# Optimization experiments

Hardware: AMD Instinct MI355X
Metric: run time of the kernel (lower is better)

## Reference

```python
import jax, jax.numpy as jnp
import numpy as np

B = 16384
OUT = 128          # output_size (per conditioning frame)
NCOND = 3
HID = 32           # MLP3 hidden
LSTM_H = 64        # lstm_output_size (input == hidden)
NPRED = 25
EPS = 1e-5


def setup_inputs() -> dict:
    key = jax.random.key(0)
    ks = jax.random.split(key, 20)
    d = {
        "x0": jax.random.normal(ks[0], (B, OUT), jnp.float32),
        "x1": jax.random.normal(ks[1], (B, OUT), jnp.float32),
        "x2": jax.random.normal(ks[2], (B, OUT), jnp.float32),
        # MLP3: Linear(384->32), BN, ReLU, Linear(32->32), BN, ReLU, Linear(32->64)
        "W1": jax.random.normal(ks[3], (HID, OUT * NCOND), jnp.float32) * 0.05,
        "b1": jnp.full((HID,), 0.03, jnp.float32),
        "g1": jnp.ones((HID,), jnp.float32),
        "beta1": jnp.zeros((HID,), jnp.float32),
        "W2": jax.random.normal(ks[4], (HID, HID), jnp.float32) * 0.1,
        "b2": jnp.full((HID,), 0.03, jnp.float32),
        "g2": jnp.ones((HID,), jnp.float32),
        "beta2": jnp.zeros((HID,), jnp.float32),
        "W3": jax.random.normal(ks[5], (LSTM_H, HID), jnp.float32) * 0.1,
        "b3": jnp.full((LSTM_H,), 0.03, jnp.float32),
        # LSTM (torch gate order i,f,g,o): weight_ih (4H,H), weight_hh (4H,H)
        "Wih": jax.random.normal(ks[6], (4 * LSTM_H, LSTM_H), jnp.float32) * 0.08,
        "Whh": jax.random.normal(ks[7], (4 * LSTM_H, LSTM_H), jnp.float32) * 0.08,
        "bih": jnp.zeros((4 * LSTM_H,), jnp.float32),
        "bhh": jnp.zeros((4 * LSTM_H,), jnp.float32),
    }
    return d


def _bn_train(h, g, b):
    # BatchNorm1d in training mode: biased batch statistics
    m = jnp.mean(h, axis=0)
    v = jnp.var(h, axis=0)
    return g * (h - m) * jax.lax.rsqrt(v + EPS) + b


def _lstm_step(inp, h, c, Wih, Whh, bih, bhh):
    gates = inp @ Wih.T + bih + h @ Whh.T + bhh  # (B, 4H)
    i, f, g, o = jnp.split(gates, 4, axis=1)
    c_new = jax.nn.sigmoid(f) * c + jax.nn.sigmoid(i) * jnp.tanh(g)
    h_new = jax.nn.sigmoid(o) * jnp.tanh(c_new)
    return h_new, c_new


def reference(x0, x1, x2, W1, b1, g1, beta1, W2, b2, g2, beta2, W3, b3,
              Wih, Whh, bih, bhh):
    x = jnp.concatenate([x0, x1, x2], axis=1)          # (B, 384)
    h = jax.nn.relu(_bn_train(x @ W1.T + b1, g1, beta1))
    h = jax.nn.relu(_bn_train(h @ W2.T + b2, g2, beta2))
    m = h @ W3.T + b3                                   # (B, 64)

    h0 = jnp.zeros((m.shape[0], LSTM_H), m.dtype)
    c0 = jnp.zeros_like(h0)
    # initial conditioning step (output discarded except as state/next input)
    h1, c1 = _lstm_step(m, h0, c0, Wih, Whh, bih, bhh)

    def step(carry, _):
        hh, cc = carry
        # loop feeds previous output back as input; output == h for 1-layer LSTM
        hn, cn = _lstm_step(hh, hh, cc, Wih, Whh, bih, bhh)
        return (hn, cn), hn

    _, outs = jax.lax.scan(step, (h1, c1), None, length=NPRED)  # (25, B, 64)
    return jnp.transpose(outs, (1, 0, 2))                        # (B, 25, 64)
```

## Files before the change

kernel.cpp:

```cpp
#include <hip/hip_runtime.h>


#define EPSV 1e-5f
#define LOG2E 1.4426950408889634f
#define K2    2.8853900817779268f

typedef __attribute__((ext_vector_type(8))) short bf16x8;
typedef __attribute__((ext_vector_type(4))) float f32x4;

__device__ __forceinline__ float rcp_f(float x) { return __builtin_amdgcn_rcpf(x); }
__device__ __forceinline__ void split_bf16(float x, ushort& hi, ushort& lo) {
    unsigned xb = __builtin_bit_cast(unsigned, x);
    hi = (ushort)(xb >> 16);
    float hif = __builtin_bit_cast(float, xb & 0xffff0000u);
    unsigned lb = __builtin_bit_cast(unsigned, x - hif);
    lo = (ushort)(lb >> 16);
}

__global__ __launch_bounds__(256) void k_prep(
    const float* __restrict__ Wih, const float* __restrict__ Whh,
    const float* __restrict__ bih, const float* __restrict__ bhh,
    const float* __restrict__ W1, const float* __restrict__ W2,
    ushort* __restrict__ Wih_hi, ushort* __restrict__ Wih_lo,
    ushort* __restrict__ Wsum_hi, ushort* __restrict__ Wsum_lo,
    ushort* __restrict__ W1hi, ushort* __restrict__ W1lo,
    ushort* __restrict__ W2hi, ushort* __restrict__ W2lo,
    float* __restrict__ bsum)
{
    int i = blockIdx.x * 256 + threadIdx.x;
    ushort h, l;
    if (i < 16384) {
        int j = i >> 6;
        float sc = (j >= 128 && j < 192) ? K2 : LOG2E;
        float wi  = Wih[i] * sc;
        float wsv = (Wih[i] + Whh[i]) * sc;
        split_bf16(wi, h, l);  Wih_hi[i] = h;  Wih_lo[i] = l;
        split_bf16(wsv, h, l); Wsum_hi[i] = h; Wsum_lo[i] = l;
    }
    if (i < 12288) { split_bf16(W1[i], h, l); W1hi[i] = h; W1lo[i] = l; }
    if (i < 1024)  { split_bf16(W2[i], h, l); W2hi[i] = h; W2lo[i] = l; }
    if (i < 256) {
        float sc = (i >= 128 && i < 192) ? K2 : LOG2E;
        bsum[i] = (bih[i] + bhh[i]) * sc;
    }
}

__global__ __launch_bounds__(256) void k_red(const float* __restrict__ part,
                                             const float* __restrict__ g,
                                             const float* __restrict__ be,
                                             float* __restrict__ scsh) {
    __shared__ float rs[256], rq[256];
    const int ch = blockIdx.x, t = threadIdx.x;
    float s = (part[t * 32 + ch] + part[(t + 256) * 32 + ch]) +
              (part[(t + 512) * 32 + ch] + part[(t + 768) * 32 + ch]);
    float q = (part[32768 + t * 32 + ch] + part[32768 + (t + 256) * 32 + ch]) +
              (part[32768 + (t + 512) * 32 + ch] + part[32768 + (t + 768) * 32 + ch]);
    rs[t] = s; rq[t] = q;
    __syncthreads();
    #pragma unroll
    for (int off = 128; off > 0; off >>= 1) {
        if (t < off) { rs[t] += rs[t + off]; rq[t] += rq[t + off]; }
        __syncthreads();
    }
    if (t == 0) {
        float mu = rs[0] * (1.f / 16384.f);
        float va = rq[0] * (1.f / 16384.f) - mu * mu;
        float sc = g[ch] * rsqrtf(va + EPSV);
        scsh[ch] = sc; scsh[32 + ch] = be[ch] - mu * sc;
    }
}

__global__ __launch_bounds__(256) void k_mlp1(
    const float* __restrict__ x0, const float* __restrict__ x1, const float* __restrict__ x2,
    const ushort* __restrict__ W1hi, const ushort* __restrict__ W1lo,
    const float* __restrict__ b1,
    float* __restrict__ pre, float* __restrict__ st1p)
{
    __shared__ __align__(16) ushort xhi[32 * 392];
    __shared__ __align__(16) ushort xlo[32 * 392];
    const int tid = threadIdx.x;
    const int r0  = blockIdx.x * 32;

    for (int a = 0; a < 3; ++a) {
        const float* xp = (a == 0) ? x0 : (a == 1) ? x1 : x2;
        const float4* src = (const float4*)(xp + (size_t)r0 * 128);
        #pragma unroll
        for (int it = 0; it < 4; ++it) {
            int i = it * 256 + tid;
            int row = i >> 5, c4 = i & 31;
            float4 v = src[i];
            ushort h0, l0, h1, l1, h2, l2, h3, l3;
            split_bf16(v.x, h0, l0); split_bf16(v.y, h1, l1);
            split_bf16(v.z, h2, l2); split_bf16(v.w, h3, l3);
            int ofs = row * 392 + a * 128 + c4 * 4;
            *(ushort4*)&xhi[ofs] = make_ushort4(h0, h1, h2, h3);
            *(ushort4*)&xlo[ofs] = make_ushort4(l0, l1, l2, l3);
        }
    }
    __syncthreads();

    const int lane = tid & 63, l15 = lane & 15, lg = lane >> 4, q = tid >> 6;
    const int m0 = (q & 1) * 16, n0 = (q >> 1) * 16;
    const float bias = b1[n0 + l15];
    f32x4 acc = {bias, bias, bias, bias};
    #pragma unroll
    for (int kt = 0; kt < 12; ++kt) {
        bf16x8 ahi = *(const bf16x8*)&xhi[(m0 + l15) * 392 + kt * 32 + lg * 8];
        bf16x8 alo = *(const bf16x8*)&xlo[(m0 + l15) * 392 + kt * 32 + lg * 8];
        bf16x8 bhi = *(const bf16x8*)(W1hi + (size_t)(n0 + l15) * 384 + kt * 32 + lg * 8);
        bf16x8 blo = *(const bf16x8*)(W1lo + (size_t)(n0 + l15) * 384 + kt * 32 + lg * 8);
        acc = __builtin_amdgcn_mfma_f32_16x16x32_bf16(ahi, bhi, acc, 0, 0, 0);
        acc = __builtin_amdgcn_mfma_f32_16x16x32_bf16(ahi, blo, acc, 0, 0, 0);
        acc = __builtin_amdgcn_mfma_f32_16x16x32_bf16(alo, bhi, acc, 0, 0, 0);
    }
    #pragma unroll
    for (int rg = 0; rg < 4; ++rg)
        pre[(size_t)(r0 + m0 + lg * 4 + rg) * 32 + n0 + l15] = acc[rg];
    float s  = (acc[0] + acc[1]) + (acc[2] + acc[3]);
    float sq = (acc[0] * acc[0] + acc[1] * acc[1]) + (acc[2] * acc[2] + acc[3] * acc[3]);
    s  += __shfl_xor(s, 16);  s  += __shfl_xor(s, 32);
    sq += __shfl_xor(sq, 16); sq += __shfl_xor(sq, 32);
    if (lg == 0) {
        int slot = (blockIdx.x * 2 + (q & 1)) * 32 + n0 + l15;
        st1p[slot] = s;
        st1p[32768 + slot] = sq;
    }
}

__global__ __launch_bounds__(256) void k_mlp2(
    float* __restrict__ pre, const float* __restrict__ scsh1,
    const ushort* __restrict__ W2hi, const ushort* __restrict__ W2lo,
    const float* __restrict__ b2, float* __restrict__ st2p)
{
    __shared__ __align__(16) ushort hhi[32 * 40];
    __shared__ __align__(16) ushort hlo[32 * 40];
    __shared__ float bnsc[32], bnsh[32];
    const int tid = threadIdx.x;
    const int r0  = blockIdx.x * 32;

    if (tid < 32) { bnsc[tid] = scsh1[tid]; bnsh[tid] = scsh1[32 + tid]; }
    __syncthreads();
    {
        int row = tid >> 3, c4 = tid & 7;
        float4 v = ((const float4*)(pre + (size_t)r0 * 32))[tid];
        float e0 = fmaxf(fmaf(v.x, bnsc[c4 * 4 + 0], bnsh[c4 * 4 + 0]), 0.f);
        float e1 = fmaxf(fmaf(v.y, bnsc[c4 * 4 + 1], bnsh[c4 * 4 + 1]), 0.f);
        float e2 = fmaxf(fmaf(v.z, bnsc[c4 * 4 + 2], bnsh[c4 * 4 + 2]), 0.f);
        float e3 = fmaxf(fmaf(v.w, bnsc[c4 * 4 + 3], bnsh[c4 * 4 + 3]), 0.f);
        ushort h0, l0, h1, l1, h2, l2, h3, l3;
        split_bf16(e0, h0, l0); split_bf16(e1, h1, l1);
        split_bf16(e2, h2, l2); split_bf16(e3, h3, l3);
        int ofs = row * 40 + c4 * 4;
        *(ushort4*)&hhi[ofs] = make_ushort4(h0, h1, h2, h3);
        *(ushort4*)&hlo[ofs] = make_ushort4(l0, l1, l2, l3);
    }
    __syncthreads();

    const int lane = tid & 63, l15 = lane & 15, lg = lane >> 4, q = tid >> 6;
    const int m0 = (q & 1) * 16, n0 = (q >> 1) * 16;
    const float bias = b2[n0 + l15];
    f32x4 acc = {bias, bias, bias, bias};
    bf16x8 ahi = *(const bf16x8*)&hhi[(m0 + l15) * 40 + lg * 8];
    bf16x8 alo = *(const bf16x8*)&hlo[(m0 + l15) * 40 + lg * 8];
    bf16x8 bhi = *(const bf16x8*)(W2hi + (size_t)(n0 + l15) * 32 + lg * 8);
    bf16x8 blo = *(const bf16x8*)(W2lo + (size_t)(n0 + l15) * 32 + lg * 8);
    acc = __builtin_amdgcn_mfma_f32_16x16x32_bf16(ahi, bhi, acc, 0, 0, 0);
    acc = __builtin_amdgcn_mfma_f32_16x16x32_bf16(ahi, blo, acc, 0, 0, 0);
    acc = __builtin_amdgcn_mfma_f32_16x16x32_bf16(alo, bhi, acc, 0, 0, 0);

    #pragma unroll
    for (int rg = 0; rg < 4; ++rg)
        pre[(size_t)(r0 + m0 + lg * 4 + rg) * 32 + n0 + l15] = acc[rg];
    float s  = (acc[0] + acc[1]) + (acc[2] + acc[3]);
    float sq = (acc[0] * acc[0] + acc[1] * acc[1]) + (acc[2] * acc[2] + acc[3] * acc[3]);
    s  += __shfl_xor(s, 16);  s  += __shfl_xor(s, 32);
    sq += __shfl_xor(sq, 16); sq += __shfl_xor(sq, 32);
    if (lg == 0) {
        int slot = (blockIdx.x * 2 + (q & 1)) * 32 + n0 + l15;
        st2p[slot] = s;
        st2p[32768 + slot] = sq;
    }
}

__global__ __launch_bounds__(256, 2) void k_lstm(
    const float* __restrict__ pre, const float* __restrict__ scsh2,
    const float* __restrict__ W3, const float* __restrict__ b3,
    const ushort* __restrict__ Wih_hi, const ushort* __restrict__ Wih_lo,
    const ushort* __restrict__ Wsum_hi, const ushort* __restrict__ Wsum_lo,
    const float* __restrict__ bsum, float* __restrict__ out)
{
    __shared__ __align__(16) ushort hhi[2][2][16][72];
    __shared__ __align__(16) ushort hlo[2][2][16][72];
    __shared__ float bn2sc[32], bn2sh[32];
    const int tid  = threadIdx.x;
    const int lane = tid & 63, l15 = lane & 15, lg = lane >> 4, q = tid >> 6;
    const int r0   = blockIdx.x * 32;

    if (tid < 32) { bn2sc[tid] = scsh2[tid]; bn2sh[tid] = scsh2[32 + tid]; }
    __syncthreads();

    {
        const int row = tid & 31, seg = tid >> 5;
        float h2[32];
        const float4* pr = (const float4*)(pre + (size_t)(r0 + row) * 32);
        #pragma unroll
        for (int j4 = 0; j4 < 8; ++j4) {
            float4 v = pr[j4];
            h2[j4 * 4 + 0] = v.x; h2[j4 * 4 + 1] = v.y;
            h2[j4 * 4 + 2] = v.z; h2[j4 * 4 + 3] = v.w;
        }
        #pragma unroll
        for (int j = 0; j < 32; ++j) h2[j] = fmaxf(fmaf(h2[j], bn2sc[j], bn2sh[j]), 0.f);
        #pragma unroll
        for (int uu = 0; uu < 8; ++uu) {
            int u = seg * 8 + uu;
            const float* w = W3 + u * 32;
            float a0 = 0.f, a1 = 0.f, a2 = 0.f, a3 = 0.f;
            #pragma unroll
            for (int k = 0; k < 32; k += 4) {
                a0 = fmaf(h2[k + 0], w[k + 0], a0);
                a1 = fmaf(h2[k + 1], w[k + 1], a1);
                a2 = fmaf(h2[k + 2], w[k + 2], a2);
                a3 = fmaf(h2[k + 3], w[k + 3], a3);
            }
            float m = b3[u] + ((a0 + a1) + (a2 + a3));
            ushort mh, ml; split_bf16(m, mh, ml);
            hhi[row >> 4][0][row & 15][u] = mh;
            hlo[row >> 4][0][row & 15][u] = ml;
        }
    }

    float bias[4];
    #pragma unroll
    for (int nt = 0; nt < 4; ++nt) bias[nt] = bsum[nt * 64 + q * 16 + l15];
    float cA[4] = {0.f, 0.f, 0.f, 0.f}, cB[4] = {0.f, 0.f, 0.f, 0.f};

    float* obA[4];
    float* obB[4];
    #pragma unroll
    for (int rg = 0; rg < 4; ++rg) {
        obA[rg] = out + (size_t)(r0 + lg * 4 + rg) * 1600 + (q * 16 + l15);
        obB[rg] = out + (size_t)(r0 + 16 + lg * 4 + rg) * 1600 + (q * 16 + l15);
    }

    bf16x8 Bhi[4][2], Blo[4][2];
    const size_t wofs = (size_t)(q * 16 + l15) * 64 + lg * 8;
    #pragma unroll
    for (int nt = 0; nt < 4; ++nt)
        #pragma unroll
        for (int kt = 0; kt < 2; ++kt) {
            Bhi[nt][kt] = *(const bf16x8*)(Wih_hi + (size_t)nt * 4096 + wofs + kt * 32);
            Blo[nt][kt] = *(const bf16x8*)(Wih_lo + (size_t)nt * 4096 + wofs + kt * 32);
        }
    __syncthreads();

#define MFMA_GATES(ACC, G, BUF)                                                  \
    {                                                                            \
        _Pragma("unroll")                                                        \
        for (int nt = 0; nt < 4; ++nt)                                           \
            ACC[nt] = (f32x4){bias[nt], bias[nt], bias[nt], bias[nt]};           \
        _Pragma("unroll")                                                        \
        for (int kt = 0; kt < 2; ++kt) {                                         \
            bf16x8 ahi = *(const bf16x8*)&hhi[G][BUF][l15][kt * 32 + lg * 8];    \
            bf16x8 alo = *(const bf16x8*)&hlo[G][BUF][l15][kt * 32 + lg * 8];    \
            _Pragma("unroll")                                                    \
            for (int nt = 0; nt < 4; ++nt) {                                     \
                ACC[nt] = __builtin_amdgcn_mfma_f32_16x16x32_bf16(ahi, Bhi[nt][kt], ACC[nt], 0, 0, 0); \
                ACC[nt] = __builtin_amdgcn_mfma_f32_16x16x32_bf16(ahi, Blo[nt][kt], ACC[nt], 0, 0, 0); \
                ACC[nt] = __builtin_amdgcn_mfma_f32_16x16x32_bf16(alo, Bhi[nt][kt], ACC[nt], 0, 0, 0); \
            }                                                                    \
        }                                                                        \
    }

#define ACT(ACC, C, G, WBUF, OB, SLOT, WRLDS)                                    \
    {                                                                            \
        const int u = q * 16 + l15;                                              \
        _Pragma("unroll")                                                        \
        for (int rg = 0; rg < 4; ++rg) {                                         \
            int row = lg * 4 + rg;                                               \
            float iv = ACC[0][rg], fv = ACC[1][rg];                              \
            float gv = ACC[2][rg], ov = ACC[3][rg];                              \
            float Af = __builtin_amdgcn_exp2f(-fv);                              \
            float Ai = __builtin_amdgcn_exp2f(-iv);                              \
            float Bg = __builtin_amdgcn_exp2f(gv);                               \
            float sig = (Bg - 1.f) * rcp_f((1.f + Ai) * (Bg + 1.f));             \
            float cc = C[rg] * rcp_f(1.f + Af) + sig;                            \
            C[rg] = cc;                                                          \
            float Ao = __builtin_amdgcn_exp2f(-ov);                              \
            float C2 = __builtin_amdgcn_exp2f(cc * K2);                          \
            float hn = (C2 - 1.f) * rcp_f((1.f + Ao) * (C2 + 1.f));              \
            if (WRLDS) {                                                         \
                ushort hh, hl; split_bf16(hn, hh, hl);                           \
                hhi[G][WBUF][row][u] = hh;                                       \
                hlo[G][WBUF][row][u] = hl;                                       \
            }                                                                    \
            if ((SLOT) >= 0)                                                     \
                OB[rg][(size_t)(SLOT) * 64] = hn;                                \
        }                                                                        \
    }

    f32x4 accA[4], accB[4];

    MFMA_GATES(accA, 0, 0);
    MFMA_GATES(accB, 1, 0);
    #pragma unroll
    for (int nt = 0; nt < 4; ++nt)
        #pragma unroll
        for (int kt = 0; kt < 2; ++kt) {
            Bhi[nt][kt] = *(const bf16x8*)(Wsum_hi + (size_t)nt * 4096 + wofs + kt * 32);
            Blo[nt][kt] = *(const bf16x8*)(Wsum_lo + (size_t)nt * 4096 + wofs + kt * 32);
        }
    ACT(accA, cA, 0, 1, obA, -1, 1);
    __syncthreads();

    #pragma unroll 1
    for (int s = 1; s <= 25; ++s) {
        const int rb = s & 1, wb = rb ^ 1;
        MFMA_GATES(accA, 0, rb);
        ACT(accB, cB, 1, rb, obB, s - 2, 1);
        __syncthreads();
        MFMA_GATES(accB, 1, rb);
        ACT(accA, cA, 0, wb, obA, s - 1, 1);
        __syncthreads();
    }
    ACT(accB, cB, 1, 0, obB, 24, 0);

#undef MFMA_GATES
#undef ACT
}

extern "C" void kernel_launch(void* const* d_in, const int* in_sizes, int n_in,
                              void* d_out, int out_size, void* d_ws, size_t ws_size,
                              hipStream_t stream) {
    const float* x0   = (const float*)d_in[0];
    const float* x1   = (const float*)d_in[1];
    const float* x2   = (const float*)d_in[2];
    const float* W1   = (const float*)d_in[3];
    const float* b1   = (const float*)d_in[4];
    const float* g1   = (const float*)d_in[5];
    const float* be1  = (const float*)d_in[6];
    const float* W2   = (const float*)d_in[7];
    const float* b2   = (const float*)d_in[8];
    const float* g2   = (const float*)d_in[9];
    const float* be2  = (const float*)d_in[10];
    const float* W3   = (const float*)d_in[11];
    const float* b3   = (const float*)d_in[12];
    const float* Wih  = (const float*)d_in[13];
    const float* Whh  = (const float*)d_in[14];
    const float* bih  = (const float*)d_in[15];
    const float* bhh  = (const float*)d_in[16];

    float* ws    = (float*)d_ws;
    float* pre   = ws;
    float* st1p  = ws + 524288;
    float* st2p  = ws + 589824;
    float* scsh1 = ws + 655360;
    float* scsh2 = ws + 655424;
    float* bsum  = ws + 655488;
    ushort* ub   = (ushort*)(ws + 655744);
    ushort* Wih_hi  = ub;
    ushort* Wih_lo  = ub + 16384;
    ushort* Wsum_hi = ub + 32768;
    ushort* Wsum_lo = ub + 49152;
    ushort* W1hi    = ub + 65536;
    ushort* W1lo    = ub + 77824;
    ushort* W2hi    = ub + 90112;
    ushort* W2lo    = ub + 91136;

    hipLaunchKernelGGL(k_prep, dim3(64), dim3(256), 0, stream,
                       Wih, Whh, bih, bhh, W1, W2,
                       Wih_hi, Wih_lo, Wsum_hi, Wsum_lo, W1hi, W1lo, W2hi, W2lo, bsum);
    hipLaunchKernelGGL(k_mlp1, dim3(512), dim3(256), 0, stream,
                       x0, x1, x2, W1hi, W1lo, b1, pre, st1p);
    hipLaunchKernelGGL(k_red, dim3(32), dim3(256), 0, stream, st1p, g1, be1, scsh1);
    hipLaunchKernelGGL(k_mlp2, dim3(512), dim3(256), 0, stream,
                       pre, scsh1, W2hi, W2lo, b2, st2p);
    hipLaunchKernelGGL(k_red, dim3(32), dim3(256), 0, stream, st2p, g2, be2, scsh2);
    hipLaunchKernelGGL(k_lstm, dim3(512), dim3(256), 0, stream,
                       pre, scsh2, W3, b3,
                       Wih_hi, Wih_lo, Wsum_hi, Wsum_lo, bsum, (float*)d_out);
}
```

Before: 87.81 us.

## Give each wave its own 16 rows and all gates to drop LSTM barriers

Restructures the LSTM kernel so each wave holds the full 256x64 recurrent weight matrix (hi/lo bf16 split) in registers as the MFMA A operand and processes 16 batch rows independently. This removes the cross-wave __syncthreads per step, since each wave only reads and writes its own LDS slice of h. The block now covers 64 rows with half as many blocks, and output stores become float4 vectors. The cost is large register pressure (64 bf16x8 weight fragments plus biases and cell state) with launch bounds lowered to 1 block per SM, and the ping-pong overlap of two row groups is lost.

```diff
diff --git a/kernel.cpp b/kernel.cpp
--- a/kernel.cpp
+++ b/kernel.cpp
@@ -182,25 +182,25 @@
     }
 }
 
-__global__ __launch_bounds__(256, 2) void k_lstm(
+__global__ __launch_bounds__(256, 1) void k_lstm(
     const float* __restrict__ pre, const float* __restrict__ scsh2,
     const float* __restrict__ W3, const float* __restrict__ b3,
     const ushort* __restrict__ Wih_hi, const ushort* __restrict__ Wih_lo,
     const ushort* __restrict__ Wsum_hi, const ushort* __restrict__ Wsum_lo,
     const float* __restrict__ bsum, float* __restrict__ out)
 {
-    __shared__ __align__(16) ushort hhi[2][2][16][72];
-    __shared__ __align__(16) ushort hlo[2][2][16][72];
+    __shared__ __align__(16) ushort Hhi[4][16][80];
+    __shared__ __align__(16) ushort Hlo[4][16][80];
     __shared__ float bn2sc[32], bn2sh[32];
     const int tid  = threadIdx.x;
-    const int lane = tid & 63, l15 = lane & 15, lg = lane >> 4, q = tid >> 6;
-    const int r0   = blockIdx.x * 32;
+    const int lane = tid & 63, l15 = lane & 15, lg = lane >> 4, w = tid >> 6;
+    const int r0   = blockIdx.x * 64;
 
     if (tid < 32) { bn2sc[tid] = scsh2[tid]; bn2sh[tid] = scsh2[32 + tid]; }
     __syncthreads();
 
     {
-        const int row = tid & 31, seg = tid >> 5;
+        const int row = tid & 63, seg = tid >> 6;
         float h2[32];
         const float4* pr = (const float4*)(pre + (size_t)(r0 + row) * 32);
         #pragma unroll
@@ -212,121 +212,106 @@
         #pragma unroll
         for (int j = 0; j < 32; ++j) h2[j] = fmaxf(fmaf(h2[j], bn2sc[j], bn2sh[j]), 0.f);
         #pragma unroll
-        for (int uu = 0; uu < 8; ++uu) {
-            int u = seg * 8 + uu;
-            const float* w = W3 + u * 32;
+        for (int uu = 0; uu < 16; ++uu) {
+            int u = seg * 16 + uu;
+            const float* wp = W3 + u * 32;
             float a0 = 0.f, a1 = 0.f, a2 = 0.f, a3 = 0.f;
             #pragma unroll
             for (int k = 0; k < 32; k += 4) {
-                a0 = fmaf(h2[k + 0], w[k + 0], a0);
-                a1 = fmaf(h2[k + 1], w[k + 1], a1);
-                a2 = fmaf(h2[k + 2], w[k + 2], a2);
-                a3 = fmaf(h2[k + 3], w[k + 3], a3);
+                a0 = fmaf(h2[k + 0], wp[k + 0], a0);
+                a1 = fmaf(h2[k + 1], wp[k + 1], a1);
+                a2 = fmaf(h2[k + 2], wp[k + 2], a2);
+                a3 = fmaf(h2[k + 3], wp[k + 3], a3);
             }
             float m = b3[u] + ((a0 + a1) + (a2 + a3));
             ushort mh, ml; split_bf16(m, mh, ml);
-            hhi[row >> 4][0][row & 15][u] = mh;
-            hlo[row >> 4][0][row & 15][u] = ml;
-        }
-    }
-
-    float bias[4];
-    #pragma unroll
-    for (int nt = 0; nt < 4; ++nt) bias[nt] = bsum[nt * 64 + q * 16 + l15];
-    float cA[4] = {0.f, 0.f, 0.f, 0.f}, cB[4] = {0.f, 0.f, 0.f, 0.f};
-
-    float* obA[4];
-    float* obB[4];
-    #pragma unroll
-    for (int rg = 0; rg < 4; ++rg) {
-        obA[rg] = out + (size_t)(r0 + lg * 4 + rg) * 1600 + (q * 16 + l15);
-        obB[rg] = out + (size_t)(r0 + 16 + lg * 4 + rg) * 1600 + (q * 16 + l15);
-    }
-
-    bf16x8 Bhi[4][2], Blo[4][2];
-    const size_t wofs = (size_t)(q * 16 + l15) * 64 + lg * 8;
-    #pragma unroll
-    for (int nt = 0; nt < 4; ++nt)
+            Hhi[row >> 4][row & 15][u] = mh;
+            Hlo[row >> 4][row & 15][u] = ml;
+        }
+    }
+
+    bf16x8 Wh[16][2], Wl[16][2];
+    const size_t afs = (size_t)l15 * 64 + lg * 8;
+    #pragma unroll
+    for (int mt = 0; mt < 16; ++mt)
         #pragma unroll
         for (int kt = 0; kt < 2; ++kt) {
-            Bhi[nt][kt] = *(const bf16x8*)(Wih_hi + (size_t)nt * 4096 + wofs + kt * 32);
-            Blo[nt][kt] = *(const bf16x8*)(Wih_lo + (size_t)nt * 4096 + wofs + kt * 32);
-        }
-    __syncthreads();
-
-#define MFMA_GATES(ACC, G, BUF)                                                  \
+            Wh[mt][kt] = *(const bf16x8*)(Wih_hi + (size_t)mt * 1024 + afs + kt * 32);
+            Wl[mt][kt] = *(const bf16x8*)(Wih_lo + (size_t)mt * 1024 + afs + kt * 32);
+        }
+    f32x4 biasv[16];
+    #pragma unroll
+    for (int mt = 0; mt < 16; ++mt) {
+        float4 bv = *(const float4*)(bsum + mt * 16 + lg * 4);
+        biasv[mt] = (f32x4){bv.x, bv.y, bv.z, bv.w};
+    }
+    float c[16];
+    #pragma unroll
+    for (int ci = 0; ci < 16; ++ci) c[ci] = 0.f;
+    float* obase = out + (size_t)(r0 + w * 16 + l15) * 1600 + lg * 4;
+
+    __syncthreads();
+
+#define STEP(SLOT)                                                               \
     {                                                                            \
-        _Pragma("unroll")                                                        \
-        for (int nt = 0; nt < 4; ++nt)                                           \
-            ACC[nt] = (f32x4){bias[nt], bias[nt], bias[nt], bias[nt]};           \
+        bf16x8 fh[2], fl[2];                                                     \
         _Pragma("unroll")                                                        \
         for (int kt = 0; kt < 2; ++kt) {                                         \
-            bf16x8 ahi = *(const bf16x8*)&hhi[G][BUF][l15][kt * 32 + lg * 8];    \
-            bf16x8 alo = *(const bf16x8*)&hlo[G][BUF][l15][kt * 32 + lg * 8];    \
+            fh[kt] = *(const bf16x8*)&Hhi[w][l15][kt * 32 + lg * 8];             \
+            fl[kt] = *(const bf16x8*)&Hlo[w][l15][kt * 32 + lg * 8];             \
+        }                                                                        \
+        _Pragma("unroll")                                                        \
+        for (int nt = 0; nt < 4; ++nt) {                                         \
+            f32x4 acc[4];                                                        \
             _Pragma("unroll")                                                    \
-            for (int nt = 0; nt < 4; ++nt) {                                     \
-                ACC[nt] = __builtin_amdgcn_mfma_f32_16x16x32_bf16(ahi, Bhi[nt][kt], ACC[nt], 0, 0, 0); \
-                ACC[nt] = __builtin_amdgcn_mfma_f32_16x16x32_bf16(ahi, Blo[nt][kt], ACC[nt], 0, 0, 0); \
-                ACC[nt] = __builtin_amdgcn_mfma_f32_16x16x32_bf16(alo, Bhi[nt][kt], ACC[nt], 0, 0, 0); \
+            for (int g = 0; g < 4; ++g) {                                        \
+                const int mt = g * 4 + nt;                                       \
+                acc[g] = biasv[mt];                                              \
+                _Pragma("unroll")                                                \
+                for (int kt = 0; kt < 2; ++kt) {                                 \
+                    acc[g] = __builtin_amdgcn_mfma_f32_16x16x32_bf16(Wh[mt][kt], fh[kt], acc[g], 0, 0, 0); \
+                    acc[g] = __builtin_amdgcn_mfma_f32_16x16x32_bf16(Wl[mt][kt], fh[kt], acc[g], 0, 0, 0); \
+                    acc[g] = __builtin_amdgcn_mfma_f32_16x16x32_bf16(Wh[mt][kt], fl[kt], acc[g], 0, 0, 0); \
+                }                                                                \
             }                                                                    \
+            ushort4 ph, pl; float4 ov;                                           \
+            _Pragma("unroll")                                                    \
+            for (int rg = 0; rg < 4; ++rg) {                                     \
+                const int ci = nt * 4 + rg;                                      \
+                float iv = acc[0][rg], fv = acc[1][rg];                          \
+                float gv = acc[2][rg], o_ = acc[3][rg];                          \
+                float Af = __builtin_amdgcn_exp2f(-fv);                          \
+                float Ai = __builtin_amdgcn_exp2f(-iv);                          \
+                float Bg = __builtin_amdgcn_exp2f(gv);                           \
+                float sig = (Bg - 1.f) * rcp_f((1.f + Ai) * (Bg + 1.f));         \
+                float cc = c[ci] * rcp_f(1.f + Af) + sig;                        \
+                c[ci] = cc;                                                      \
+                float Ao = __builtin_amdgcn_exp2f(-o_);                          \
+                float C2 = __builtin_amdgcn_exp2f(cc * K2);                      \
+                float hn = (C2 - 1.f) * rcp_f((1.f + Ao) * (C2 + 1.f));          \
+                ushort hh, hl; split_bf16(hn, hh, hl);                           \
+                ((ushort*)&ph)[rg] = hh; ((ushort*)&pl)[rg] = hl;                \
+                ((float*)&ov)[rg] = hn;                                          \
+            }                                                                    \
+            *(ushort4*)&Hhi[w][l15][nt * 16 + lg * 4] = ph;                      \
+            *(ushort4*)&Hlo[w][l15][nt * 16 + lg * 4] = pl;                      \
+            if ((SLOT) >= 0)                                                     \
+                *(float4*)(obase + (size_t)(SLOT) * 64 + nt * 16) = ov;          \
         }                                                                        \
     }
 
-#define ACT(ACC, C, G, WBUF, OB, SLOT, WRLDS)                                    \
-    {                                                                            \
-        const int u = q * 16 + l15;                                              \
-        _Pragma("unroll")                                                        \
-        for (int rg = 0; rg < 4; ++rg) {                                         \
-            int row = lg * 4 + rg;                                               \
-            float iv = ACC[0][rg], fv = ACC[1][rg];                              \
-            float gv = ACC[2][rg], ov = ACC[3][rg];                              \
-            float Af = __builtin_amdgcn_exp2f(-fv);                              \
-            float Ai = __builtin_amdgcn_exp2f(-iv);                              \
-            float Bg = __builtin_amdgcn_exp2f(gv);                               \
-            float sig = (Bg - 1.f) * rcp_f((1.f + Ai) * (Bg + 1.f));             \
-            float cc = C[rg] * rcp_f(1.f + Af) + sig;                            \
-            C[rg] = cc;                                                          \
-            float Ao = __builtin_amdgcn_exp2f(-ov);                              \
-            float C2 = __builtin_amdgcn_exp2f(cc * K2);                          \
-            float hn = (C2 - 1.f) * rcp_f((1.f + Ao) * (C2 + 1.f));              \
-            if (WRLDS) {                                                         \
-                ushort hh, hl; split_bf16(hn, hh, hl);                           \
-                hhi[G][WBUF][row][u] = hh;                                       \
-                hlo[G][WBUF][row][u] = hl;                                       \
-            }                                                                    \
-            if ((SLOT) >= 0)                                                     \
-                OB[rg][(size_t)(SLOT) * 64] = hn;                                \
-        }                                                                        \
-    }
-
-    f32x4 accA[4], accB[4];
-
-    MFMA_GATES(accA, 0, 0);
-    MFMA_GATES(accB, 1, 0);
-    #pragma unroll
-    for (int nt = 0; nt < 4; ++nt)
+    STEP(-1);
+    #pragma unroll
+    for (int mt = 0; mt < 16; ++mt)
         #pragma unroll
         for (int kt = 0; kt < 2; ++kt) {
-            Bhi[nt][kt] = *(const bf16x8*)(Wsum_hi + (size_t)nt * 4096 + wofs + kt * 32);
-            Blo[nt][kt] = *(const bf16x8*)(Wsum_lo + (size_t)nt * 4096 + wofs + kt * 32);
-        }
-    ACT(accA, cA, 0, 1, obA, -1, 1);
-    __syncthreads();
-
+            Wh[mt][kt] = *(const bf16x8*)(Wsum_hi + (size_t)mt * 1024 + afs + kt * 32);
+            Wl[mt][kt] = *(const bf16x8*)(Wsum_lo + (size_t)mt * 1024 + afs + kt * 32);
+        }
     #pragma unroll 1
-    for (int s = 1; s <= 25; ++s) {
-        const int rb = s & 1, wb = rb ^ 1;
-        MFMA_GATES(accA, 0, rb);
-        ACT(accB, cB, 1, rb, obB, s - 2, 1);
-        __syncthreads();
-        MFMA_GATES(accB, 1, rb);
-        ACT(accA, cA, 0, wb, obA, s - 1, 1);
-        __syncthreads();
-    }
-    ACT(accB, cB, 1, 0, obB, 24, 0);
-
-#undef MFMA_GATES
-#undef ACT
+    for (int s = 1; s <= 25; ++s) STEP(s - 1);
+
+#undef STEP
 }
 
 extern "C" void kernel_launch(void* const* d_in, const int* in_sizes, int n_in,
@@ -376,7 +361,7 @@
     hipLaunchKernelGGL(k_mlp2, dim3(512), dim3(256), 0, stream,
                        pre, scsh1, W2hi, W2lo, b2, st2p);
     hipLaunchKernelGGL(k_red, dim3(32), dim3(256), 0, stream, st2p, g2, be2, scsh2);
-    hipLaunchKernelGGL(k_lstm, dim3(512), dim3(256), 0, stream,
+    hipLaunchKernelGGL(k_lstm, dim3(256), dim3(256), 0, stream,
                        pre, scsh2, W3, b3,
                        Wih_hi, Wih_lo, Wsum_hi, Wsum_lo, bsum, (float*)d_out);
 }
```

Measured after the change: 100.6 us. 14.6% more time.
